# Optimization experiments

Measured on AMD Instinct MI355X. Metric: run time of the kernel, lower is better.

Reference implementation:

```python
import jax, jax.numpy as jnp
import numpy as np

N_USERS = 100_000
N_ITEMS = 50_000
N = N_USERS + N_ITEMS  # total nodes in the normalized UI adjacency
D = 128                # emb_size == hyper_size
NNZ = 1_500_000        # nonzeros in sparse_norm_adj (COO)
EPS = 1e-5             # torch.nn.LayerNorm default eps


def setup_inputs() -> dict:
    key = jax.random.key(0)
    k1, k2, k3, k4 = jax.random.split(key, 4)
    return {
        "ego_embeddings": jax.random.normal(k1, (N, D), dtype=jnp.float32),
        "adj_vals": jax.random.uniform(k2, (NNZ,), dtype=jnp.float32),
        "ln_gamma": jnp.ones((D,), dtype=jnp.float32),
        "ln_beta": jnp.zeros((D,), dtype=jnp.float32),
        "adj_rows": jax.random.randint(k3, (NNZ,), 0, N, dtype=jnp.int32),
        "adj_cols": jax.random.randint(k4, (NNZ,), 0, N, dtype=jnp.int32),
    }


def _layer_norm(x, gamma, beta):
    mu = jnp.mean(x, axis=-1, keepdims=True)
    var = jnp.var(x, axis=-1, keepdims=True)
    return (x - mu) * jax.lax.rsqrt(var + EPS) * gamma + beta


def reference(ego_embeddings, adj_vals, ln_gamma, ln_beta, adj_rows, adj_cols):
    # HGCNConv with act=False: adj @ (adj.T @ embs), adj sparse COO [N, N]
    # (A^T @ x)[c] = sum_{(r,c) in nnz} vals * x[r]
    h = jax.ops.segment_sum(adj_vals[:, None] * ego_embeddings[adj_rows], adj_cols, num_segments=N)
    # (A @ h)[r] = sum_{(r,c) in nnz} vals * h[c]
    h2 = jax.ops.segment_sum(adj_vals[:, None] * h[adj_cols], adj_rows, num_segments=N)
    # LayerNorm + residual (last-layer branch of LocalAwareEncoder.forward)
    out = _layer_norm(h2, ln_gamma, ln_beta) + ego_embeddings
    user_all_embeddings = out[:N_USERS]
    item_all_embeddings = out[N_USERS:]
    return user_all_embeddings, item_all_embeddings
```

## Files before the change

### kernel.cpp

```cpp
#include <hip/hip_runtime.h>

#define N_TOTAL 150000
#define DIM 128
#define NNZ_E 1500000
#define NBUCK 256
#define DPB 586
#define EPB2 2048
#define A2_BLOCKS ((NNZ_E + EPB2 - 1) / EPB2)

typedef unsigned long long u64;
typedef unsigned uvec16 __attribute__((ext_vector_type(16)));
typedef unsigned uvec2  __attribute__((ext_vector_type(2)));

__device__ __forceinline__ unsigned pack_bf16_bits(unsigned ua, unsigned ub) {
    ua = (ua + 0x7FFFu + ((ua >> 16) & 1u)) >> 16;
    ub = (ub + 0x7FFFu + ((ub >> 16) & 1u)) >> 16;
    return ua | (ub << 16);
}
__device__ __forceinline__ unsigned pack_bf16(float a, float b) {
    return pack_bf16_bits(__float_as_uint(a), __float_as_uint(b));
}
__device__ __forceinline__ float2 unpack_bf16(unsigned u) {
    return make_float2(__uint_as_float(u << 16), __uint_as_float(u & 0xFFFF0000u));
}
__device__ __forceinline__ float rdlane_f(float x, int l) {
    return __uint_as_float((unsigned)__builtin_amdgcn_readlane((int)__float_as_uint(x), l));
}

__device__ __forceinline__ void sload_pair(uvec16 &a, uvec16 &b, const void* p) {
    asm volatile("s_load_dwordx16 %0, %2, 0x0\n\t"
                 "s_load_dwordx16 %1, %2, 0x40\n\t"
                 "s_waitcnt lgkmcnt(0)"
                 : "=&s"(a), "=&s"(b) : "s"(p) : "memory");
}
__device__ __forceinline__ void sload_be(uvec2 &r, const void* p) {
    asm volatile("s_load_dwordx2 %0, %1, 0x0\n\t"
                 "s_waitcnt lgkmcnt(0)"
                 : "=&s"(r) : "s"(p) : "memory");
}

__device__ __forceinline__ void chunk8(const uvec16 &m, int lim, int lane,
                                       const uint* __restrict__ srcBf,
                                       float &ax, float &ay, float &bx, float &by) {
    #pragma unroll
    for (int j = 0; j < 8; j++) {
        unsigned sx = m[2 * j] & 0x3FFFFu;
        sx = (sx < (unsigned)N_TOTAL) ? sx : 0u;
        float vv = (j < lim) ? __uint_as_float(m[2 * j + 1]) : 0.0f;
        const uint* p = srcBf + ((size_t)sx << 6);
        float2 uu = unpack_bf16(p[lane]);
        if (j & 1) { bx += vv * uu.x; by += vv * uu.y; }
        else       { ax += vv * uu.x; ay += vv * uu.y; }
    }
}

__global__ __launch_bounds__(256) void conv_bf16(const float* __restrict__ in,
                                                 uint* __restrict__ outp) {
    int i = blockIdx.x * 256 + threadIdx.x;
    const u64* in8 = (const u64*)in;
    u64 w0 = __builtin_nontemporal_load(&in8[4 * i + 0]);
    u64 w1 = __builtin_nontemporal_load(&in8[4 * i + 1]);
    u64 w2 = __builtin_nontemporal_load(&in8[4 * i + 2]);
    u64 w3 = __builtin_nontemporal_load(&in8[4 * i + 3]);
    uint4 o;
    o.x = pack_bf16_bits((unsigned)w0, (unsigned)(w0 >> 32));
    o.y = pack_bf16_bits((unsigned)w1, (unsigned)(w1 >> 32));
    o.z = pack_bf16_bits((unsigned)w2, (unsigned)(w2 >> 32));
    o.w = pack_bf16_bits((unsigned)w3, (unsigned)(w3 >> 32));
    ((uint4*)outp)[i] = o;
}

__global__ __launch_bounds__(256) void coarse_hist(const int* __restrict__ rows,
                                                   const int* __restrict__ cols,
                                                   int* __restrict__ cnt1,
                                                   int* __restrict__ cnt2) {
    __shared__ int h[512];
    int t = threadIdx.x;
    h[t] = 0; h[t + 256] = 0;
    __syncthreads();
    int stride = gridDim.x * blockDim.x;
    for (int e = blockIdx.x * blockDim.x + t; e < NNZ_E; e += stride) {
        atomicAdd(&h[cols[e] / DPB], 1);
        atomicAdd(&h[256 + rows[e] / DPB], 1);
    }
    __syncthreads();
    if (h[t]) atomicAdd(&cnt1[t], h[t]);
    if (h[t + 256]) atomicAdd(&cnt2[t], h[t + 256]);
}

__global__ __launch_bounds__(256) void scan_buckets(const int* __restrict__ cnt,
                                                    int* __restrict__ sb,
                                                    int* __restrict__ gc) {
    __shared__ int buf[256];
    int t = threadIdx.x;
    int v = cnt[t]; buf[t] = v; __syncthreads();
    for (int o = 1; o < 256; o <<= 1) {
        int a = (t >= o) ? buf[t - o] : 0; __syncthreads();
        buf[t] += a; __syncthreads();
    }
    sb[t] = buf[t] - v;
    __syncthreads();
    int v2 = cnt[256 + t]; buf[t] = v2; __syncthreads();
    for (int o = 1; o < 256; o <<= 1) {
        int a = (t >= o) ? buf[t - o] : 0; __syncthreads();
        buf[t] += a; __syncthreads();
    }
    sb[256 + t] = NNZ_E + buf[t] - v2;
    if (t == 255) sb[512] = 2 * NNZ_E;
    gc[t] = 0; gc[256 + t] = 0;
}

__global__ __launch_bounds__(256) void phaseA_fused(const int* __restrict__ rows,
                                                    const int* __restrict__ cols,
                                                    const float* __restrict__ vals,
                                                    const int* __restrict__ slabBase,
                                                    int* __restrict__ gCur,
                                                    uint2* __restrict__ slab) {
    __shared__ uint2 sortedL[2 * EPB2];
    __shared__ unsigned short bktL[2 * EPB2];
    __shared__ int cnt[512], off[512], cur[512], gbase[512];
    __shared__ int part[256];
    __shared__ int totE;
    int t = threadIdx.x;
    int base = blockIdx.x * EPB2;
    cnt[t] = 0; cnt[t + 256] = 0;
    __syncthreads();

    uint2 eA[8], eB[8];
    short bA[8], bB[8];
    #pragma unroll
    for (int j = 0; j < 8; j++) {
        int e = base + j * 256 + t;
        if (e < NNZ_E) {
            int r = rows[e], c = cols[e];
            unsigned v = __float_as_uint(vals[e]);
            int b1 = c / DPB, dl1 = c - b1 * DPB;
            int b2 = r / DPB, dl2 = r - b2 * DPB;
            bA[j] = (short)b1;
            eA[j].x = ((unsigned)dl1 << 18) | (unsigned)r;
            eA[j].y = v;
            bB[j] = (short)(256 + b2);
            eB[j].x = ((unsigned)dl2 << 18) | (unsigned)c;
            eB[j].y = v;
            atomicAdd(&cnt[b1], 1);
            atomicAdd(&cnt[256 + b2], 1);
        } else { bA[j] = -1; bB[j] = -1; }
    }
    __syncthreads();
    int c0 = cnt[2 * t], c1 = cnt[2 * t + 1];
    int ps = c0 + c1;
    part[t] = ps; __syncthreads();
    for (int o = 1; o < 256; o <<= 1) {
        int a = (t >= o) ? part[t - o] : 0; __syncthreads();
        part[t] += a; __syncthreads();
    }
    int bs = part[t] - ps;
    off[2 * t] = bs;          cur[2 * t] = bs;
    off[2 * t + 1] = bs + c0; cur[2 * t + 1] = bs + c0;
    if (t == 255) totE = part[255];
    __syncthreads();
    #pragma unroll
    for (int j = 0; j < 8; j++) {
        if (bA[j] >= 0) {
            int p = atomicAdd(&cur[(int)bA[j]], 1);
            sortedL[p] = eA[j]; bktL[p] = (unsigned short)bA[j];
            p = atomicAdd(&cur[(int)bB[j]], 1);
            sortedL[p] = eB[j]; bktL[p] = (unsigned short)bB[j];
        }
    }
    __syncthreads();
    for (int b = t; b < 512; b += 256) {
        int n = cnt[b];
        if (n > 0) gbase[b] = atomicAdd(&gCur[b], n);
    }
    __syncthreads();
    int nE = totE;
    for (int i = t; i < nE; i += 256) {
        int b = bktL[i];
        slab[slabBase[b] + gbase[b] + (i - off[b])] = sortedL[i];
    }
}

__global__ __launch_bounds__(256) void phaseB(const uint2* __restrict__ slab,
                                              const int* __restrict__ slabBase,
                                              int* __restrict__ offs1,
                                              int* __restrict__ offs2,
                                              uint2* __restrict__ sorted) {
    __shared__ int cnt[DPB], sc[DPB], cur[DPB], part[256];
    int b = blockIdx.x, t = threadIdx.x;
    int sb = slabBase[b], se = slabBase[b + 1];
    int n = se - sb;
    for (int d = t; d < DPB; d += 256) cnt[d] = 0;
    __syncthreads();
    for (int i = t; i < n; i += 256)
        atomicAdd(&cnt[slab[sb + i].x >> 18], 1);
    __syncthreads();
    int d0 = t * 3;
    int c0 = (d0     < DPB) ? cnt[d0]     : 0;
    int c1 = (d0 + 1 < DPB) ? cnt[d0 + 1] : 0;
    int c2 = (d0 + 2 < DPB) ? cnt[d0 + 2] : 0;
    int ps = c0 + c1 + c2;
    part[t] = ps;
    __syncthreads();
    for (int o = 1; o < 256; o <<= 1) {
        int a = (t >= o) ? part[t - o] : 0; __syncthreads();
        part[t] += a; __syncthreads();
    }
    int bs = part[t] - ps;
    if (d0     < DPB) { sc[d0]     = bs;           cur[d0]     = bs; }
    if (d0 + 1 < DPB) { sc[d0 + 1] = bs + c0;      cur[d0 + 1] = bs + c0; }
    if (d0 + 2 < DPB) { sc[d0 + 2] = bs + c0 + c1; cur[d0 + 2] = bs + c0 + c1; }
    __syncthreads();
    int destBase = (b & 255) * DPB;
    int* offs = (b < NBUCK) ? offs1 : offs2;
    for (int d = t; d < DPB; d += 256) {
        int dd = destBase + d;
        if (dd <= N_TOTAL) offs[dd] = sb + sc[d];
    }
    for (int i = t; i < n; i += 256) {
        uint2 e = slab[sb + i];
        int dl = e.x >> 18;
        int p = atomicAdd(&cur[dl], 1);
        sorted[sb + p] = make_uint2(e.x & 0x3FFFF, e.y);
    }
}

__global__ __launch_bounds__(256) void gather1(const uint* __restrict__ srcBf,
                                               const int* __restrict__ offs,
                                               const uint2* __restrict__ edges,
                                               uint* __restrict__ dstBf) {
    int lane = threadIdx.x & 63;
    int row = blockIdx.x * 4 + (threadIdx.x >> 6);
    int row_u = __builtin_amdgcn_readfirstlane(row);
    uvec2 be;
    sload_be(be, offs + row_u);
    int beg = (int)be[0];
    int n = (int)be[1] - beg;
    const u64* ep = (const u64*)edges + beg;
    uvec16 mA, mB;
    sload_pair(mA, mB, ep);
    float ax = 0.f, ay = 0.f, bx = 0.f, by = 0.f;
    chunk8(mA, n < 8 ? n : 8, lane, srcBf, ax, ay, bx, by);
    if (n > 8) {
        chunk8(mB, n - 8 < 8 ? n - 8 : 8, lane, srcBf, ax, ay, bx, by);
        if (n > 16) {
            uvec16 mC, mD;
            sload_pair(mC, mD, ep + 16);
            chunk8(mC, n - 16 < 8 ? n - 16 : 8, lane, srcBf, ax, ay, bx, by);
            if (n > 24) {
                chunk8(mD, n - 24 < 8 ? n - 24 : 8, lane, srcBf, ax, ay, bx, by);
                for (int k = 32; k < n; k++) {
                    uint2 e = edges[beg + k];
                    float v = __uint_as_float(e.y);
                    float2 u = unpack_bf16(srcBf[(((size_t)e.x) << 6) + lane]);
                    ax += v * u.x; ay += v * u.y;
                }
            }
        }
    }
    dstBf[(size_t)row_u * 64 + lane] = pack_bf16(ax + bx, ay + by);
}

__global__ __launch_bounds__(256) void gather2_ln(const uint* __restrict__ hBf,
                                                  const int* __restrict__ offs,
                                                  const uint2* __restrict__ edges,
                                                  const uint* __restrict__ egoBf,
                                                  const float* __restrict__ gamma,
                                                  const float* __restrict__ beta,
                                                  float* __restrict__ out) {
    int lane = threadIdx.x & 63;
    int row = blockIdx.x * 4 + (threadIdx.x >> 6);
    int row_u = __builtin_amdgcn_readfirstlane(row);
    uvec2 be;
    sload_be(be, offs + row_u);
    int beg = (int)be[0];
    int n = (int)be[1] - beg;
    const u64* ep = (const u64*)edges + beg;
    uvec16 mA, mB;
    sload_pair(mA, mB, ep);
    float ax = 0.f, ay = 0.f, bx = 0.f, by = 0.f;
    chunk8(mA, n < 8 ? n : 8, lane, hBf, ax, ay, bx, by);
    if (n > 8) {
        chunk8(mB, n - 8 < 8 ? n - 8 : 8, lane, hBf, ax, ay, bx, by);
        if (n > 16) {
            uvec16 mC, mD;
            sload_pair(mC, mD, ep + 16);
            chunk8(mC, n - 16 < 8 ? n - 16 : 8, lane, hBf, ax, ay, bx, by);
            if (n > 24) {
                chunk8(mD, n - 24 < 8 ? n - 24 : 8, lane, hBf, ax, ay, bx, by);
                for (int k = 32; k < n; k++) {
                    uint2 e = edges[beg + k];
                    float v = __uint_as_float(e.y);
                    float2 u = unpack_bf16(hBf[(((size_t)e.x) << 6) + lane]);
                    ax += v * u.x; ay += v * u.y;
                }
            }
        }
    }
    float2 acc = make_float2(ax + bx, ay + by);
    float s = acc.x + acc.y;
    float sq = acc.x * acc.x + acc.y * acc.y;
    #pragma unroll
    for (int o = 1; o <= 16; o <<= 1) {
        s  += __shfl_xor(s, o, 64);
        sq += __shfl_xor(sq, o, 64);
    }
    float sT  = rdlane_f(s, 0)  + rdlane_f(s, 32);
    float sqT = rdlane_f(sq, 0) + rdlane_f(sq, 32);
    float mu = sT * (1.0f / DIM);
    float var = sqT * (1.0f / DIM) - mu * mu;
    float rs = rsqrtf(var + 1e-5f);
    float2 g  = ((const float2*)gamma)[lane];
    float2 bb = ((const float2*)beta)[lane];
    unsigned egoW = __builtin_nontemporal_load(&egoBf[(size_t)row_u * 64 + lane]);
    float2 e2 = unpack_bf16(egoW);
    float2 o2;
    o2.x = (acc.x - mu) * rs * g.x + bb.x + e2.x;
    o2.y = (acc.y - mu) * rs * g.y + bb.y + e2.y;
    u64 ow = (u64)__float_as_uint(o2.x) | ((u64)__float_as_uint(o2.y) << 32);
    __builtin_nontemporal_store(ow, (u64*)out + (size_t)row_u * 64 + lane);
}

__device__ __forceinline__ void atomic_add_f32(float* p, float v) {
    __hip_atomic_fetch_add(p, v, __ATOMIC_RELAXED, __HIP_MEMORY_SCOPE_AGENT);
}
__global__ void scatter_kernel(const float* __restrict__ src, const float* __restrict__ vals,
                               const int* __restrict__ gidx, const int* __restrict__ sidx,
                               float* __restrict__ dst, int nnz) {
    int gid = blockIdx.x * blockDim.x + threadIdx.x;
    int e = gid >> 5, lane = gid & 31;
    if (e >= nnz) return;
    float v = vals[e];
    float4 x = ((const float4*)(src + (size_t)gidx[e] * DIM))[lane];
    float* d = dst + (size_t)sidx[e] * DIM + lane * 4;
    atomic_add_f32(d + 0, v * x.x); atomic_add_f32(d + 1, v * x.y);
    atomic_add_f32(d + 2, v * x.z); atomic_add_f32(d + 3, v * x.w);
}
__global__ void ln_residual_kernel(const float* __restrict__ h2, const float* __restrict__ ego,
                                   const float* __restrict__ gamma, const float* __restrict__ beta,
                                   float* __restrict__ out, int nrows) {
    int gid = blockIdx.x * blockDim.x + threadIdx.x;
    int row = gid >> 6, lane = gid & 63;
    if (row >= nrows) return;
    float2 x = ((const float2*)(h2 + (size_t)row * DIM))[lane];
    float s = x.x + x.y, sq = x.x * x.x + x.y * x.y;
    #pragma unroll
    for (int o = 32; o > 0; o >>= 1) { s += __shfl_xor(s, o, 64); sq += __shfl_xor(sq, o, 64); }
    float mu = s * (1.0f / DIM), var = sq * (1.0f / DIM) - mu * mu;
    float rs = rsqrtf(var + 1e-5f);
    float2 eg = ((const float2*)(ego + (size_t)row * DIM))[lane];
    float2 g = ((const float2*)gamma)[lane], b = ((const float2*)beta)[lane];
    float2 o2;
    o2.x = (x.x - mu) * rs * g.x + b.x + eg.x;
    o2.y = (x.y - mu) * rs * g.y + b.y + eg.y;
    ((float2*)(out + (size_t)row * DIM))[lane] = o2;
}

extern "C" void kernel_launch(void* const* d_in, const int* in_sizes, int n_in,
                              void* d_out, int out_size, void* d_ws, size_t ws_size,
                              hipStream_t stream) {
    const float* ego   = (const float*)d_in[0];
    const float* vals  = (const float*)d_in[1];
    const float* gamma = (const float*)d_in[2];
    const float* beta  = (const float*)d_in[3];
    const int*   rows  = (const int*)d_in[4];
    const int*   cols  = (const int*)d_in[5];
    float* out = (float*)d_out;

    const size_t EGO_BF_B = (size_t)N_TOTAL * DIM * 2;
    const size_t SLAB_B   = (size_t)2 * NNZ_E * sizeof(uint2);
    const size_t H_BF_B   = (size_t)N_TOTAL * DIM * 2;
    const size_t REGION_B = (SLAB_B > H_BF_B) ? SLAB_B : H_BF_B;
    const size_t SORT_B   = (size_t)2 * NNZ_E * sizeof(uint2);
    const size_t OFFS_B   = ((size_t)N_TOTAL + 16) * sizeof(int);
    const size_t SMALL    = 16384;
    const size_t REQ = EGO_BF_B + REGION_B + SORT_B + 2 * OFFS_B + SMALL;
    const size_t H_FP32_B = (size_t)N_TOTAL * DIM * sizeof(float);

    char* w = (char*)d_ws;
    uint* egoBf   = (uint*)w;   w += EGO_BF_B;
    char* region  = w;          w += REGION_B;
    uint2* slab   = (uint2*)region;
    uint* hBf     = (uint*)region;
    uint2* sorted = (uint2*)w;  w += SORT_B;
    int* offs1    = (int*)w;    w += OFFS_B;
    int* offs2    = (int*)w;    w += OFFS_B;
    int* cntArr   = (int*)w;    w += 512 * sizeof(int);
    int* sb       = (int*)w;    w += 516 * sizeof(int);
    int* gc       = (int*)w;    w += 512 * sizeof(int);

    if (ws_size >= REQ) {
        (void)hipMemsetAsync(cntArr, 0, 512 * sizeof(int), stream);
        conv_bf16<<<(N_TOTAL * DIM / 8) / 256, 256, 0, stream>>>(ego, egoBf);
        coarse_hist<<<512, 256, 0, stream>>>(rows, cols, cntArr, cntArr + 256);
        scan_buckets<<<1, 256, 0, stream>>>(cntArr, sb, gc);
        phaseA_fused<<<A2_BLOCKS, 256, 0, stream>>>(rows, cols, vals, sb, gc, slab);
        phaseB<<<512, 256, 0, stream>>>(slab, sb, offs1, offs2, sorted);

        int ggrid = (N_TOTAL + 3) / 4;
        gather1<<<ggrid, 256, 0, stream>>>(egoBf, offs1, sorted, hBf);
        gather2_ln<<<ggrid, 256, 0, stream>>>(hBf, offs2, sorted, egoBf, gamma, beta, out);
    } else {
        float* h = (float*)d_ws;
        (void)hipMemsetAsync(h, 0, H_FP32_B, stream);
        (void)hipMemsetAsync(out, 0, H_FP32_B, stream);
        long total = (long)NNZ_E * 32;
        int grid = (int)((total + 255) / 256);
        scatter_kernel<<<grid, 256, 0, stream>>>(ego, vals, rows, cols, h, NNZ_E);
        scatter_kernel<<<grid, 256, 0, stream>>>(h, vals, cols, rows, out, NNZ_E);
        int lngrid = (N_TOTAL * 64 + 255) / 256;
        ln_residual_kernel<<<lngrid, 256, 0, stream>>>(out, ego, gamma, beta, out, N_TOTAL);
    }
}
```

Before: 369.8 us.

## Replace two-pass bucket sort with padded per-row ELL table and overflow list

Drops the coarse histogram, bucket scan and two-phase counting sort that built a CSR edge list. Each row now gets a fixed 20-slot padded table filled by global atomics on per-row counters, and edges beyond 20 go to a small global overflow list that the gather kernels scan linearly. The table is rebuilt between the two gathers so one buffer serves both directions. This trades the sort passes for random global atomics and scattered writes. With about 10 edges per row, some rows will exceed 20 and trigger a scan of the whole overflow list, which is silently dropped past 4096 entries.

```diff
diff --git a/kernel.cpp b/kernel.cpp
--- a/kernel.cpp
+++ b/kernel.cpp
@@ -3,14 +3,13 @@
 #define N_TOTAL 150000
 #define DIM 128
 #define NNZ_E 1500000
-#define NBUCK 256
-#define DPB 586
-#define EPB2 2048
-#define A2_BLOCKS ((NNZ_E + EPB2 - 1) / EPB2)
+#define PAD 20
+#define ROW_B 160
+#define OVF_CAP 4096
 
 typedef unsigned long long u64;
 typedef unsigned uvec16 __attribute__((ext_vector_type(16)));
-typedef unsigned uvec2  __attribute__((ext_vector_type(2)));
+typedef unsigned uvec8  __attribute__((ext_vector_type(8)));
 
 __device__ __forceinline__ unsigned pack_bf16_bits(unsigned ua, unsigned ub) {
     ua = (ua + 0x7FFFu + ((ua >> 16) & 1u)) >> 16;
@@ -27,16 +26,15 @@
     return __uint_as_float((unsigned)__builtin_amdgcn_readlane((int)__float_as_uint(x), l));
 }
 
-__device__ __forceinline__ void sload_pair(uvec16 &a, uvec16 &b, const void* p) {
-    asm volatile("s_load_dwordx16 %0, %2, 0x0\n\t"
-                 "s_load_dwordx16 %1, %2, 0x40\n\t"
+__device__ __forceinline__ void sload_row20(uvec16 &a, uvec16 &b, uvec8 &c, unsigned &n,
+                                            const void* tp, const void* cp) {
+    asm volatile("s_load_dwordx16 %0, %4, 0x0\n\t"
+                 "s_load_dwordx16 %1, %4, 0x40\n\t"
+                 "s_load_dwordx8 %2, %4, 0x80\n\t"
+                 "s_load_dword %3, %5, 0x0\n\t"
                  "s_waitcnt lgkmcnt(0)"
-                 : "=&s"(a), "=&s"(b) : "s"(p) : "memory");
-}
-__device__ __forceinline__ void sload_be(uvec2 &r, const void* p) {
-    asm volatile("s_load_dwordx2 %0, %1, 0x0\n\t"
-                 "s_waitcnt lgkmcnt(0)"
-                 : "=&s"(r) : "s"(p) : "memory");
+                 : "=&s"(a), "=&s"(b), "=&s"(c), "=&s"(n)
+                 : "s"(tp), "s"(cp) : "memory");
 }
 
 __device__ __forceinline__ void chunk8(const uvec16 &m, int lim, int lane,
@@ -44,6 +42,20 @@
                                        float &ax, float &ay, float &bx, float &by) {
     #pragma unroll
     for (int j = 0; j < 8; j++) {
+        unsigned sx = m[2 * j] & 0x3FFFFu;
+        sx = (sx < (unsigned)N_TOTAL) ? sx : 0u;
+        float vv = (j < lim) ? __uint_as_float(m[2 * j + 1]) : 0.0f;
+        const uint* p = srcBf + ((size_t)sx << 6);
+        float2 uu = unpack_bf16(p[lane]);
+        if (j & 1) { bx += vv * uu.x; by += vv * uu.y; }
+        else       { ax += vv * uu.x; ay += vv * uu.y; }
+    }
+}
+__device__ __forceinline__ void chunk4(const uvec8 &m, int lim, int lane,
+                                       const uint* __restrict__ srcBf,
+                                       float &ax, float &ay, float &bx, float &by) {
+    #pragma unroll
+    for (int j = 0; j < 4; j++) {
         unsigned sx = m[2 * j] & 0x3FFFFu;
         sx = (sx < (unsigned)N_TOTAL) ? sx : 0u;
         float vv = (j < lim) ? __uint_as_float(m[2 * j + 1]) : 0.0f;
@@ -70,190 +82,54 @@
     ((uint4*)outp)[i] = o;
 }
 
-__global__ __launch_bounds__(256) void coarse_hist(const int* __restrict__ rows,
-                                                   const int* __restrict__ cols,
-                                                   int* __restrict__ cnt1,
-                                                   int* __restrict__ cnt2) {
-    __shared__ int h[512];
-    int t = threadIdx.x;
-    h[t] = 0; h[t + 256] = 0;
-    __syncthreads();
+__global__ __launch_bounds__(256) void build_table(const int* __restrict__ dsts,
+                                                   const int* __restrict__ srcs,
+                                                   const float* __restrict__ vals,
+                                                   int* __restrict__ cnt,
+                                                   u64* __restrict__ table,
+                                                   int* __restrict__ ovfCnt,
+                                                   uint4* __restrict__ ovf) {
     int stride = gridDim.x * blockDim.x;
-    for (int e = blockIdx.x * blockDim.x + t; e < NNZ_E; e += stride) {
-        atomicAdd(&h[cols[e] / DPB], 1);
-        atomicAdd(&h[256 + rows[e] / DPB], 1);
-    }
-    __syncthreads();
-    if (h[t]) atomicAdd(&cnt1[t], h[t]);
-    if (h[t + 256]) atomicAdd(&cnt2[t], h[t + 256]);
-}
-
-__global__ __launch_bounds__(256) void scan_buckets(const int* __restrict__ cnt,
-                                                    int* __restrict__ sb,
-                                                    int* __restrict__ gc) {
-    __shared__ int buf[256];
-    int t = threadIdx.x;
-    int v = cnt[t]; buf[t] = v; __syncthreads();
-    for (int o = 1; o < 256; o <<= 1) {
-        int a = (t >= o) ? buf[t - o] : 0; __syncthreads();
-        buf[t] += a; __syncthreads();
-    }
-    sb[t] = buf[t] - v;
-    __syncthreads();
-    int v2 = cnt[256 + t]; buf[t] = v2; __syncthreads();
-    for (int o = 1; o < 256; o <<= 1) {
-        int a = (t >= o) ? buf[t - o] : 0; __syncthreads();
-        buf[t] += a; __syncthreads();
-    }
-    sb[256 + t] = NNZ_E + buf[t] - v2;
-    if (t == 255) sb[512] = 2 * NNZ_E;
-    gc[t] = 0; gc[256 + t] = 0;
-}
-
-__global__ __launch_bounds__(256) void phaseA_fused(const int* __restrict__ rows,
-                                                    const int* __restrict__ cols,
-                                                    const float* __restrict__ vals,
-                                                    const int* __restrict__ slabBase,
-                                                    int* __restrict__ gCur,
-                                                    uint2* __restrict__ slab) {
-    __shared__ uint2 sortedL[2 * EPB2];
-    __shared__ unsigned short bktL[2 * EPB2];
-    __shared__ int cnt[512], off[512], cur[512], gbase[512];
-    __shared__ int part[256];
-    __shared__ int totE;
-    int t = threadIdx.x;
-    int base = blockIdx.x * EPB2;
-    cnt[t] = 0; cnt[t + 256] = 0;
-    __syncthreads();
-
-    uint2 eA[8], eB[8];
-    short bA[8], bB[8];
-    #pragma unroll
-    for (int j = 0; j < 8; j++) {
-        int e = base + j * 256 + t;
-        if (e < NNZ_E) {
-            int r = rows[e], c = cols[e];
-            unsigned v = __float_as_uint(vals[e]);
-            int b1 = c / DPB, dl1 = c - b1 * DPB;
-            int b2 = r / DPB, dl2 = r - b2 * DPB;
-            bA[j] = (short)b1;
-            eA[j].x = ((unsigned)dl1 << 18) | (unsigned)r;
-            eA[j].y = v;
-            bB[j] = (short)(256 + b2);
-            eB[j].x = ((unsigned)dl2 << 18) | (unsigned)c;
-            eB[j].y = v;
-            atomicAdd(&cnt[b1], 1);
-            atomicAdd(&cnt[256 + b2], 1);
-        } else { bA[j] = -1; bB[j] = -1; }
-    }
-    __syncthreads();
-    int c0 = cnt[2 * t], c1 = cnt[2 * t + 1];
-    int ps = c0 + c1;
-    part[t] = ps; __syncthreads();
-    for (int o = 1; o < 256; o <<= 1) {
-        int a = (t >= o) ? part[t - o] : 0; __syncthreads();
-        part[t] += a; __syncthreads();
-    }
-    int bs = part[t] - ps;
-    off[2 * t] = bs;          cur[2 * t] = bs;
-    off[2 * t + 1] = bs + c0; cur[2 * t + 1] = bs + c0;
-    if (t == 255) totE = part[255];
-    __syncthreads();
-    #pragma unroll
-    for (int j = 0; j < 8; j++) {
-        if (bA[j] >= 0) {
-            int p = atomicAdd(&cur[(int)bA[j]], 1);
-            sortedL[p] = eA[j]; bktL[p] = (unsigned short)bA[j];
-            p = atomicAdd(&cur[(int)bB[j]], 1);
-            sortedL[p] = eB[j]; bktL[p] = (unsigned short)bB[j];
+    for (int e = blockIdx.x * blockDim.x + threadIdx.x; e < NNZ_E; e += stride) {
+        int d = dsts[e], s = srcs[e];
+        unsigned v = __float_as_uint(vals[e]);
+        int slot = atomicAdd(&cnt[d], 1);
+        if (slot < PAD) {
+            table[(size_t)d * PAD + slot] = (u64)(unsigned)s | ((u64)v << 32);
+        } else {
+            int o = atomicAdd(ovfCnt, 1);
+            if (o < OVF_CAP) ovf[o] = make_uint4((unsigned)d, (unsigned)s, v, 0u);
         }
     }
-    __syncthreads();
-    for (int b = t; b < 512; b += 256) {
-        int n = cnt[b];
-        if (n > 0) gbase[b] = atomicAdd(&gCur[b], n);
-    }
-    __syncthreads();
-    int nE = totE;
-    for (int i = t; i < nE; i += 256) {
-        int b = bktL[i];
-        slab[slabBase[b] + gbase[b] + (i - off[b])] = sortedL[i];
-    }
-}
-
-__global__ __launch_bounds__(256) void phaseB(const uint2* __restrict__ slab,
-                                              const int* __restrict__ slabBase,
-                                              int* __restrict__ offs1,
-                                              int* __restrict__ offs2,
-                                              uint2* __restrict__ sorted) {
-    __shared__ int cnt[DPB], sc[DPB], cur[DPB], part[256];
-    int b = blockIdx.x, t = threadIdx.x;
-    int sb = slabBase[b], se = slabBase[b + 1];
-    int n = se - sb;
-    for (int d = t; d < DPB; d += 256) cnt[d] = 0;
-    __syncthreads();
-    for (int i = t; i < n; i += 256)
-        atomicAdd(&cnt[slab[sb + i].x >> 18], 1);
-    __syncthreads();
-    int d0 = t * 3;
-    int c0 = (d0     < DPB) ? cnt[d0]     : 0;
-    int c1 = (d0 + 1 < DPB) ? cnt[d0 + 1] : 0;
-    int c2 = (d0 + 2 < DPB) ? cnt[d0 + 2] : 0;
-    int ps = c0 + c1 + c2;
-    part[t] = ps;
-    __syncthreads();
-    for (int o = 1; o < 256; o <<= 1) {
-        int a = (t >= o) ? part[t - o] : 0; __syncthreads();
-        part[t] += a; __syncthreads();
-    }
-    int bs = part[t] - ps;
-    if (d0     < DPB) { sc[d0]     = bs;           cur[d0]     = bs; }
-    if (d0 + 1 < DPB) { sc[d0 + 1] = bs + c0;      cur[d0 + 1] = bs + c0; }
-    if (d0 + 2 < DPB) { sc[d0 + 2] = bs + c0 + c1; cur[d0 + 2] = bs + c0 + c1; }
-    __syncthreads();
-    int destBase = (b & 255) * DPB;
-    int* offs = (b < NBUCK) ? offs1 : offs2;
-    for (int d = t; d < DPB; d += 256) {
-        int dd = destBase + d;
-        if (dd <= N_TOTAL) offs[dd] = sb + sc[d];
-    }
-    for (int i = t; i < n; i += 256) {
-        uint2 e = slab[sb + i];
-        int dl = e.x >> 18;
-        int p = atomicAdd(&cur[dl], 1);
-        sorted[sb + p] = make_uint2(e.x & 0x3FFFF, e.y);
-    }
 }
 
 __global__ __launch_bounds__(256) void gather1(const uint* __restrict__ srcBf,
-                                               const int* __restrict__ offs,
-                                               const uint2* __restrict__ edges,
+                                               const int* __restrict__ cnt,
+                                               const u64* __restrict__ table,
+                                               const int* __restrict__ ovfCnt,
+                                               const uint4* __restrict__ ovf,
                                                uint* __restrict__ dstBf) {
     int lane = threadIdx.x & 63;
     int row = blockIdx.x * 4 + (threadIdx.x >> 6);
     int row_u = __builtin_amdgcn_readfirstlane(row);
-    uvec2 be;
-    sload_be(be, offs + row_u);
-    int beg = (int)be[0];
-    int n = (int)be[1] - beg;
-    const u64* ep = (const u64*)edges + beg;
-    uvec16 mA, mB;
-    sload_pair(mA, mB, ep);
+    uvec16 mA, mB; uvec8 mC; unsigned nu;
+    sload_row20(mA, mB, mC, nu, (const char*)table + (size_t)row_u * ROW_B, cnt + row_u);
+    int n = (int)nu;
     float ax = 0.f, ay = 0.f, bx = 0.f, by = 0.f;
     chunk8(mA, n < 8 ? n : 8, lane, srcBf, ax, ay, bx, by);
     if (n > 8) {
         chunk8(mB, n - 8 < 8 ? n - 8 : 8, lane, srcBf, ax, ay, bx, by);
         if (n > 16) {
-            uvec16 mC, mD;
-            sload_pair(mC, mD, ep + 16);
-            chunk8(mC, n - 16 < 8 ? n - 16 : 8, lane, srcBf, ax, ay, bx, by);
-            if (n > 24) {
-                chunk8(mD, n - 24 < 8 ? n - 24 : 8, lane, srcBf, ax, ay, bx, by);
-                for (int k = 32; k < n; k++) {
-                    uint2 e = edges[beg + k];
-                    float v = __uint_as_float(e.y);
-                    float2 u = unpack_bf16(srcBf[(((size_t)e.x) << 6) + lane]);
-                    ax += v * u.x; ay += v * u.y;
+            chunk4(mC, n - 16 < 4 ? n - 16 : 4, lane, srcBf, ax, ay, bx, by);
+            if (n > PAD) {
+                int oc = *ovfCnt; oc = oc < OVF_CAP ? oc : OVF_CAP;
+                for (int i = 0; i < oc; i++) {
+                    uint4 e = ovf[i];
+                    if (e.x == (unsigned)row_u) {
+                        float v = __uint_as_float(e.z);
+                        float2 u = unpack_bf16(srcBf[(((size_t)e.y) << 6) + lane]);
+                        ax += v * u.x; ay += v * u.y;
+                    }
                 }
             }
         }
@@ -262,8 +138,10 @@
 }
 
 __global__ __launch_bounds__(256) void gather2_ln(const uint* __restrict__ hBf,
-                                                  const int* __restrict__ offs,
-                                                  const uint2* __restrict__ edges,
+                                                  const int* __restrict__ cnt,
+                                                  const u64* __restrict__ table,
+                                                  const int* __restrict__ ovfCnt,
+                                                  const uint4* __restrict__ ovf,
                                                   const uint* __restrict__ egoBf,
                                                   const float* __restrict__ gamma,
                                                   const float* __restrict__ beta,
@@ -271,28 +149,24 @@
     int lane = threadIdx.x & 63;
     int row = blockIdx.x * 4 + (threadIdx.x >> 6);
     int row_u = __builtin_amdgcn_readfirstlane(row);
-    uvec2 be;
-    sload_be(be, offs + row_u);
-    int beg = (int)be[0];
-    int n = (int)be[1] - beg;
-    const u64* ep = (const u64*)edges + beg;
-    uvec16 mA, mB;
-    sload_pair(mA, mB, ep);
+    uvec16 mA, mB; uvec8 mC; unsigned nu;
+    sload_row20(mA, mB, mC, nu, (const char*)table + (size_t)row_u * ROW_B, cnt + row_u);
+    int n = (int)nu;
     float ax = 0.f, ay = 0.f, bx = 0.f, by = 0.f;
     chunk8(mA, n < 8 ? n : 8, lane, hBf, ax, ay, bx, by);
     if (n > 8) {
         chunk8(mB, n - 8 < 8 ? n - 8 : 8, lane, hBf, ax, ay, bx, by);
         if (n > 16) {
-            uvec16 mC, mD;
-            sload_pair(mC, mD, ep + 16);
-            chunk8(mC, n - 16 < 8 ? n - 16 : 8, lane, hBf, ax, ay, bx, by);
-            if (n > 24) {
-                chunk8(mD, n - 24 < 8 ? n - 24 : 8, lane, hBf, ax, ay, bx, by);
-                for (int k = 32; k < n; k++) {
-                    uint2 e = edges[beg + k];
-                    float v = __uint_as_float(e.y);
-                    float2 u = unpack_bf16(hBf[(((size_t)e.x) << 6) + lane]);
-                    ax += v * u.x; ay += v * u.y;
+            chunk4(mC, n - 16 < 4 ? n - 16 : 4, lane, hBf, ax, ay, bx, by);
+            if (n > PAD) {
+                int oc = *ovfCnt; oc = oc < OVF_CAP ? oc : OVF_CAP;
+                for (int i = 0; i < oc; i++) {
+                    uint4 e = ovf[i];
+                    if (e.x == (unsigned)row_u) {
+                        float v = __uint_as_float(e.z);
+                        float2 u = unpack_bf16(hBf[(((size_t)e.y) << 6) + lane]);
+                        ax += v * u.x; ay += v * u.y;
+                    }
                 }
             }
         }
@@ -368,38 +242,35 @@
     float* out = (float*)d_out;
 
     const size_t EGO_BF_B = (size_t)N_TOTAL * DIM * 2;
-    const size_t SLAB_B   = (size_t)2 * NNZ_E * sizeof(uint2);
     const size_t H_BF_B   = (size_t)N_TOTAL * DIM * 2;
-    const size_t REGION_B = (SLAB_B > H_BF_B) ? SLAB_B : H_BF_B;
-    const size_t SORT_B   = (size_t)2 * NNZ_E * sizeof(uint2);
-    const size_t OFFS_B   = ((size_t)N_TOTAL + 16) * sizeof(int);
-    const size_t SMALL    = 16384;
-    const size_t REQ = EGO_BF_B + REGION_B + SORT_B + 2 * OFFS_B + SMALL;
+    const size_t TABLE_B  = (size_t)N_TOTAL * PAD * 8;
+    const size_t CNT_B    = (size_t)150016 * sizeof(int);
+    const size_t OVFC_B   = 256;
+    const size_t OVF_B    = (size_t)OVF_CAP * 16;
+    const size_t REQ = EGO_BF_B + H_BF_B + TABLE_B + 2 * CNT_B + OVFC_B + 2 * OVF_B;
     const size_t H_FP32_B = (size_t)N_TOTAL * DIM * sizeof(float);
 
     char* w = (char*)d_ws;
     uint* egoBf   = (uint*)w;   w += EGO_BF_B;
-    char* region  = w;          w += REGION_B;
-    uint2* slab   = (uint2*)region;
-    uint* hBf     = (uint*)region;
-    uint2* sorted = (uint2*)w;  w += SORT_B;
-    int* offs1    = (int*)w;    w += OFFS_B;
-    int* offs2    = (int*)w;    w += OFFS_B;
-    int* cntArr   = (int*)w;    w += 512 * sizeof(int);
-    int* sb       = (int*)w;    w += 516 * sizeof(int);
-    int* gc       = (int*)w;    w += 512 * sizeof(int);
+    uint* hBf     = (uint*)w;   w += H_BF_B;
+    u64*  table   = (u64*)w;    w += TABLE_B;
+    int*  cnt1    = (int*)w;    w += CNT_B;
+    int*  cnt2    = (int*)w;    w += CNT_B;
+    int*  ovfc    = (int*)w;    w += OVFC_B;
+    uint4* ovf1   = (uint4*)w;  w += OVF_B;
+    uint4* ovf2   = (uint4*)w;  w += OVF_B;
 
     if (ws_size >= REQ) {
-        (void)hipMemsetAsync(cntArr, 0, 512 * sizeof(int), stream);
+        (void)hipMemsetAsync(cnt1, 0, 2 * CNT_B + OVFC_B, stream);
         conv_bf16<<<(N_TOTAL * DIM / 8) / 256, 256, 0, stream>>>(ego, egoBf);
-        coarse_hist<<<512, 256, 0, stream>>>(rows, cols, cntArr, cntArr + 256);
-        scan_buckets<<<1, 256, 0, stream>>>(cntArr, sb, gc);
-        phaseA_fused<<<A2_BLOCKS, 256, 0, stream>>>(rows, cols, vals, sb, gc, slab);
-        phaseB<<<512, 256, 0, stream>>>(slab, sb, offs1, offs2, sorted);
-
-        int ggrid = (N_TOTAL + 3) / 4;
-        gather1<<<ggrid, 256, 0, stream>>>(egoBf, offs1, sorted, hBf);
-        gather2_ln<<<ggrid, 256, 0, stream>>>(hBf, offs2, sorted, egoBf, gamma, beta, out);
+
+        build_table<<<2048, 256, 0, stream>>>(cols, rows, vals, cnt1, table, ovfc, ovf1);
+        int ggrid = N_TOTAL / 4;
+        gather1<<<ggrid, 256, 0, stream>>>(egoBf, cnt1, table, ovfc, ovf1, hBf);
+
+        build_table<<<2048, 256, 0, stream>>>(rows, cols, vals, cnt2, table, ovfc + 32, ovf2);
+        gather2_ln<<<ggrid, 256, 0, stream>>>(hBf, cnt2, table, ovfc + 32, ovf2,
+                                              egoBf, gamma, beta, out);
     } else {
         float* h = (float*)d_ws;
         (void)hipMemsetAsync(h, 0, H_FP32_B, stream);
```

Measured after the change: 522.7 us. +41.4%, slower.
